# Kernel tuning notes

Hardware: AMD Instinct MI355X
Metric: run time of the kernel (lower is better)

Reference implementation:

```python
import jax, jax.numpy as jnp
import numpy as np

NUM_NODES = 2048
NUM_UNITS = 64
INPUT_DIM = 2
MAX_K = 2  # max_diffusion_step


def setup_inputs() -> dict:
    key = jax.random.key(0)
    ks = jax.random.split(key, 8)
    B, N, U, D = 32, NUM_NODES, NUM_UNITS, INPUT_DIM
    C = D + U                      # input_size after concat = 66
    M = 2 * MAX_K + 1              # num_matrices = 5
    w_scale = 1.0 / np.sqrt(C * M)
    return {
        "inputs": jax.random.normal(ks[0], (B, N * D), dtype=jnp.float32),
        "hx": jax.random.normal(ks[1], (B, N * U), dtype=jnp.float32),
        # row-stochastic-ish random-walk supports (scaled so K hops stay bounded)
        "support0": jax.random.uniform(ks[2], (N, N), dtype=jnp.float32) / N,
        "support1": jax.random.uniform(ks[3], (N, N), dtype=jnp.float32) / N,
        "W_ru": jax.random.normal(ks[4], (C * M, 2 * U), dtype=jnp.float32) * w_scale,
        "b_ru": jnp.full((2 * U,), 1.0, dtype=jnp.float32),   # bias_start=1.0
        "W_c": jax.random.normal(ks[5], (C * M, U), dtype=jnp.float32) * w_scale,
        "b_c": jnp.zeros((U,), dtype=jnp.float32),            # bias_start=0.0
    }


def _gconv(inputs, state, supports, W, b, output_size):
    # inputs: [B, N*D], state: [B, N*U]
    B = inputs.shape[0]
    N = NUM_NODES
    x0 = jnp.concatenate(
        [inputs.reshape(B, N, -1), state.reshape(B, N, -1)], axis=2
    )  # [B, N, C]
    C = x0.shape[2]
    xs = [x0]
    for S in supports:  # Chebyshev-style diffusion per support
        x1 = jnp.einsum("nm,bmc->bnc", S, x0)
        xs.append(x1)
        xk1, xk2 = x1, x0
        for _ in range(2, MAX_K + 1):
            x2 = 2.0 * jnp.einsum("nm,bmc->bnc", S, xk1) - xk2
            xs.append(x2)
            xk1, xk2 = x2, xk1
    M = len(xs)  # num_matrices
    # stack on new leading axis then permute(1,2,3,0): feature-major, matrix-minor
    x = jnp.stack(xs, axis=0).transpose(1, 2, 3, 0).reshape(B * N, C * M)
    out = x @ W + b  # [B*N, output_size]
    return out.reshape(B, N * output_size)


def reference(inputs, hx, support0, support1, W_ru, b_ru, W_c, b_c):
    B = inputs.shape[0]
    N, U = NUM_NODES, NUM_UNITS
    supports = (support0, support1)
    value = jax.nn.sigmoid(_gconv(inputs, hx, supports, W_ru, b_ru, 2 * U))
    value = value.reshape(B, N, 2 * U)
    r = value[..., :U].reshape(B, N * U)
    u = value[..., U:].reshape(B, N * U)
    c = jnp.tanh(_gconv(inputs, r * hx, supports, W_c, b_c, U))
    new_state = u * hx + (1.0 - u) * c
    return new_state
```

## Files before the change

kernel.cpp:

```cpp
#include <hip/hip_runtime.h>
#include <hip/hip_bf16.h>
#include <cstdint>
#include <cstddef>

typedef unsigned short u16;
typedef unsigned char u8;
using f32x4 = __attribute__((ext_vector_type(4))) float;
using s16x8 = __attribute__((ext_vector_type(8))) short;
using s64x2 = __attribute__((ext_vector_type(2))) long;

#define NN 2048
#define BB 32
#define CC 66
#define JREAL 2112
#define JR 2176
#define KF 352
#define SROWS 65536

__device__ __forceinline__ int kperm(int k6) {
  return 16 * ((k6 >> 3) & 3) + 8 * (k6 >> 5) + (k6 & 7);
}

__device__ __forceinline__ float bf2f(u16 u) {
  union { uint32_t i; float f; } v; v.i = ((uint32_t)u) << 16; return v.f;
}
__device__ __forceinline__ u16 f2bf(float f) {
  union { float f; uint32_t i; } v; v.f = f;
  uint32_t x = v.i;
  x += 0x7fffu + ((x >> 16) & 1u);
  return (u16)(x >> 16);
}
__device__ __forceinline__ u8 f2e4m3(float x) {
  union { float f; uint32_t i; } v; v.f = x;
  uint32_t s = (v.i >> 24) & 0x80u;
  float a = fabsf(x);
  if (a >= 464.0f) return (u8)(s | 0x7Eu);
  if (a < 0.015625f) {
    int q = (int)rintf(a * 512.0f);
    return (u8)(s | (uint32_t)q);
  }
  union { float f; uint32_t i; } u; u.f = a;
  uint32_t lsb = (u.i >> 20) & 1u;
  u.i += 0x0007FFFFu + lsb;
  int e = (int)(u.i >> 23) - 127;
  uint32_t m = (u.i >> 20) & 7u;
  return (u8)(s | ((uint32_t)(e + 7) << 3) | m);
}

__device__ __forceinline__ void async_cp16(const u8* g, u8* l) {
  __builtin_amdgcn_global_load_lds(
      (const __attribute__((address_space(1))) unsigned int*)g,
      (__attribute__((address_space(3))) unsigned int*)l, 16, 0, 0);
}
__device__ __forceinline__ void async_cp16u(const u16* g, u16* l) {
  __builtin_amdgcn_global_load_lds(
      (const __attribute__((address_space(1))) unsigned int*)g,
      (__attribute__((address_space(3))) unsigned int*)l, 16, 0, 0);
}

template <int EPI>
__global__ __launch_bounds__(512, 2) void gemm_f8(
    const u8* __restrict__ A0, const u8* __restrict__ A1,
    const u8* __restrict__ A2, const u8* __restrict__ A3,
    const u8* __restrict__ B0, const u8* __restrict__ B1,
    const u8* __restrict__ B2, const u8* __restrict__ B3,
    void* __restrict__ C0, void* __restrict__ C1,
    void* __restrict__ C2, void* __restrict__ C3,
    int K, int lda, int ldb, int ldout, int mlimit)
{
  __shared__ u8 lds[3 * 24576];

  const int gx = gridDim.x, gy = gridDim.y;
  const int nwg = gx * gy * gridDim.z;
  const int orig = blockIdx.x + gx * (blockIdx.y + gy * blockIdx.z);
  const int cpx = nwg >> 3;
  const int swz = (orig & 7) * cpx + (orig >> 3);
  const int mb = swz % gx;
  const int t1 = swz / gx;
  const int nb = t1 % gy;
  const int zb = t1 / gy;

  const u8* A = (zb == 0) ? A0 : (zb == 1) ? A1 : (zb == 2) ? A2 : A3;
  const u8* B = (zb == 0) ? B0 : (zb == 1) ? B1 : (zb == 2) ? B2 : B3;
  void* Cv    = (zb == 0) ? C0 : (zb == 1) ? C1 : (zb == 2) ? C2 : C3;

  const int tid = threadIdx.x;
  const int wid = tid >> 6;
  const int lane = tid & 63;
  const int m0 = mb * 128;
  const int n0 = nb * 256;
  const int wm = (wid >> 2) * 64;
  const int wn = (wid & 3) * 64;

  const int srow = wid * 16 + (lane >> 2);
  const int sk   = ((lane & 3) ^ ((lane >> 3) & 3)) * 16;
  const u8* gA = A + (size_t)(m0 + srow) * lda + sk;
  const u8* gB = B + (size_t)(n0 + srow) * ldb + sk;
  u8* ldsA  = &lds[wid * 1024];
  u8* ldsB0 = &lds[8192 + wid * 1024];
  u8* ldsB1 = &lds[16384 + wid * 1024];

  const int r16 = lane & 15;
  const int hi = lane >> 4;
  const int rq = (r16 >> 1) & 3;
  const int goff = (hi ^ rq) * 16;
  const int abase = (wm + r16) * 64 + goff;
  const int bbase = 8192 + (wn + r16) * 64 + goff;

  f32x4 acc[4][4] = {};
  const int nt = K >> 6;

#define STAGE(T_, SO_) { const int k0_ = (T_) * 64;                          \
    async_cp16(gA + k0_, ldsA + (SO_));                                      \
    async_cp16(gB + k0_, ldsB0 + (SO_));                                     \
    async_cp16(gB + (size_t)128 * ldb + k0_, ldsB1 + (SO_)); }

  STAGE(0, 0);
  STAGE(1, 24576);
  asm volatile("s_waitcnt vmcnt(3)" ::: "memory");
  __builtin_amdgcn_s_barrier();

  int scur = 0;
  for (int t = 0; t < nt; ++t) {
    const int soff = scur * 24576;
    const bool more = (t + 2) < nt;
    if (more) {
      int sst = scur + 2; if (sst >= 3) sst -= 3;
      STAGE(t + 2, sst * 24576);
    }
    s64x2 af[4], bfr[4];
#pragma unroll
    for (int mi = 0; mi < 4; ++mi)
      af[mi] = *(const s64x2*)&lds[soff + abase + mi * 1024];
#pragma unroll
    for (int ni = 0; ni < 4; ++ni)
      bfr[ni] = *(const s64x2*)&lds[soff + bbase + ni * 1024];
    __builtin_amdgcn_s_setprio(1);
#pragma unroll
    for (int h = 0; h < 2; ++h)
#pragma unroll
      for (int mi = 0; mi < 4; ++mi)
#pragma unroll
        for (int ni = 0; ni < 4; ++ni)
          acc[mi][ni] = __builtin_amdgcn_mfma_f32_16x16x32_fp8_fp8(
              af[mi][h], bfr[ni][h], acc[mi][ni], 0, 0, 0);
    __builtin_amdgcn_s_setprio(0);
    if (more) { asm volatile("s_waitcnt vmcnt(3)" ::: "memory"); }
    else      { asm volatile("s_waitcnt vmcnt(0)" ::: "memory"); }
    __builtin_amdgcn_s_barrier();
    scur = (scur + 1 == 3) ? 0 : scur + 1;
  }
#undef STAGE

  const int lr = (lane >> 4) * 4;
  const int lc = lane & 15;

  if (EPI == 5) {
    u16* tl = (u16*)lds;
    u16* xc = (u16*)Cv;
#pragma unroll
    for (int half = 0; half < 2; ++half) {
      __syncthreads();
      if ((wn >> 7) == half) {
#pragma unroll
        for (int mi = 0; mi < 4; ++mi)
#pragma unroll
          for (int ni = 0; ni < 4; ++ni) {
            const int np = (wn & 127) + ni * 16 + lc;
#pragma unroll
            for (int r = 0; r < 4; ++r) {
              const int j = wm + mi * 16 + lr + r;
              tl[np * 130 + j] = f2bf(acc[mi][ni][r] * 0.00390625f);
            }
          }
      }
      __syncthreads();
      for (int p = 0; p < 32; ++p) {
        const int idx = p * 512 + tid;
        const int jj = idx & 127;
        const int np = idx >> 7;
        const int j = m0 + jj;
        if (j < JREAL) {
          const int b = j / CC;
          const int c = j - b * CC;
          const int ng = n0 + half * 128 + np;
          xc[((size_t)b * NN + ng) * KF + (size_t)(zb + 1) * CC + c] =
              tl[np * 130 + jj];
        }
      }
    }
  } else {
#pragma unroll
    for (int mi = 0; mi < 4; ++mi)
#pragma unroll
      for (int ni = 0; ni < 4; ++ni) {
        const int colg = n0 + wn + ni * 16 + lc;
#pragma unroll
        for (int r = 0; r < 4; ++r) {
          const int rowg = m0 + wm + mi * 16 + lr + r;
          if (rowg < mlimit) {
            if (EPI == 0) {
              ((u16*)Cv)[(size_t)rowg * ldout + colg] =
                  f2bf(acc[mi][ni][r] * 0.00390625f);
            } else {
              float v = acc[mi][ni][r] * 0.0078125f -
                        ((rowg == colg) ? 256.0f : 0.0f);
              const int cpk = (colg & ~63) + kperm(colg & 63);
              ((u8*)Cv)[(size_t)rowg * ldout + cpk] = f2e4m3(v);
            }
          }
        }
      }
  }
}

__global__ __launch_bounds__(512, 2) void gemm_f8T(
    const u8* __restrict__ A0, const u8* __restrict__ A1,
    const u8* __restrict__ B0, const u8* __restrict__ B1,
    u8* __restrict__ C0, u8* __restrict__ C1,
    int K, int lda, int ldb, int ldout)
{
  __shared__ u8 lds[3 * 16384];

  const int gx = gridDim.x, gy = gridDim.y;
  const int nwg = gx * gy * gridDim.z;
  const int orig = blockIdx.x + gx * (blockIdx.y + gy * blockIdx.z);
  const int cpx = nwg >> 3;
  const int swz = (orig & 7) * cpx + (orig >> 3);
  const int mb = swz % gx;
  const int t1 = swz / gx;
  const int nb = t1 % gy;
  const int zb = t1 / gy;

  const u8* A = zb ? A1 : A0;
  const u8* B = zb ? B1 : B0;
  u8* C = zb ? C1 : C0;

  const int tid = threadIdx.x;
  const int wid = tid >> 6;
  const int lane = tid & 63;
  const int m0 = mb * 128;
  const int n0 = nb * 128;
  const int wm = (wid >> 2) * 64;
  const int wn = (wid & 3) * 32;

  const int srow = wid * 16 + (lane >> 2);
  const int sk   = ((lane & 3) ^ ((lane >> 3) & 3)) * 16;
  const u8* gA = A + (size_t)(m0 + srow) * lda + sk;
  const u8* gB = B + (size_t)(n0 + srow) * ldb + sk;
  u8* ldsA = &lds[wid * 1024];
  u8* ldsB = &lds[8192 + wid * 1024];

  const int r16 = lane & 15;
  const int hi = lane >> 4;
  const int rq = (r16 >> 1) & 3;
  const int goff = (hi ^ rq) * 16;
  const int abase = (wm + r16) * 64 + goff;
  const int bbase = 8192 + (wn + r16) * 64 + goff;

  f32x4 acc[4][2] = {};
  const int nt = K >> 6;

#define STAGE(T_, SO_) { const int k0_ = (T_) * 64;                          \
    async_cp16(gA + k0_, ldsA + (SO_));                                      \
    async_cp16(gB + k0_, ldsB + (SO_)); }

  STAGE(0, 0);
  STAGE(1, 16384);
  asm volatile("s_waitcnt vmcnt(2)" ::: "memory");
  __builtin_amdgcn_s_barrier();

  int scur = 0;
  for (int t = 0; t < nt; ++t) {
    const int soff = scur * 16384;
    const bool more = (t + 2) < nt;
    if (more) {
      int sst = scur + 2; if (sst >= 3) sst -= 3;
      STAGE(t + 2, sst * 16384);
    }
    s64x2 af[4], bfr[2];
#pragma unroll
    for (int mi = 0; mi < 4; ++mi)
      af[mi] = *(const s64x2*)&lds[soff + abase + mi * 1024];
#pragma unroll
    for (int ni = 0; ni < 2; ++ni)
      bfr[ni] = *(const s64x2*)&lds[soff + bbase + ni * 1024];
    __builtin_amdgcn_s_setprio(1);
#pragma unroll
    for (int h = 0; h < 2; ++h)
#pragma unroll
      for (int mi = 0; mi < 4; ++mi)
#pragma unroll
        for (int ni = 0; ni < 2; ++ni)
          acc[mi][ni] = __builtin_amdgcn_mfma_f32_16x16x32_fp8_fp8(
              af[mi][h], bfr[ni][h], acc[mi][ni], 0, 0, 0);
    __builtin_amdgcn_s_setprio(0);
    if (more) { asm volatile("s_waitcnt vmcnt(2)" ::: "memory"); }
    else      { asm volatile("s_waitcnt vmcnt(0)" ::: "memory"); }
    __builtin_amdgcn_s_barrier();
    scur = (scur + 1 == 3) ? 0 : scur + 1;
  }
#undef STAGE

  const int lr = (lane >> 4) * 4;
  const int lc = lane & 15;
#pragma unroll
  for (int mi = 0; mi < 4; ++mi)
#pragma unroll
    for (int ni = 0; ni < 2; ++ni) {
      const int colg = n0 + wn + ni * 16 + lc;
      const int cpk = (colg & ~63) + kperm(colg & 63);
#pragma unroll
      for (int r = 0; r < 4; ++r) {
        const int rowg = m0 + wm + mi * 16 + lr + r;
        float v = acc[mi][ni][r] * 0.0078125f -
                  ((rowg == colg) ? 256.0f : 0.0f);
        C[(size_t)rowg * ldout + cpk] = f2e4m3(v);
      }
    }
}

template <int EPI>
__global__ __launch_bounds__(256) void gemm_dense(
    const u16* __restrict__ A, const u16* __restrict__ B, u16* __restrict__ C,
    const float* __restrict__ bias,
    int K, int lda, int ldb, int ldout, int nstore)
{
  __shared__ u16 At[128 * 32];
  __shared__ u16 Bt[128 * 32];
  const int nwg = gridDim.x;
  const int orig = blockIdx.x;
  const int cpx = nwg >> 3;
  const int swz = (orig & 7) * cpx + (orig >> 3);
  const int mb = swz;

  const int tid = threadIdx.x;
  const int wid = tid >> 6;
  const int lane = tid & 63;
  const int m0 = mb * 128;
  const int wm = (wid >> 1) * 64;
  const int wn = (wid & 1) * 64;
  const int rA = lane >> 2;
  const int kA = ((lane & 3) ^ ((lane >> 3) & 3)) * 8;

  f32x4 acc[4][4] = {};

  const int c0 = wid * 2, c1 = wid * 2 + 1;
  const u16* gA0 = A + (size_t)(m0 + c0 * 16 + rA) * lda + kA;
  const u16* gA1 = A + (size_t)(m0 + c1 * 16 + rA) * lda + kA;
  const u16* gB0 = B + (size_t)(c0 * 16 + rA) * ldb + kA;
  const u16* gB1 = B + (size_t)(c1 * 16 + rA) * ldb + kA;

  for (int k0 = 0; k0 < K; k0 += 32) {
    async_cp16u(gA0 + k0, &At[c0 * 512]);
    async_cp16u(gA1 + k0, &At[c1 * 512]);
    async_cp16u(gB0 + k0, &Bt[c0 * 512]);
    async_cp16u(gB1 + k0, &Bt[c1 * 512]);
    __syncthreads();
    s16x8 af[4], bfr[4];
    const int r16 = lane & 15;
    const int cswz = ((lane >> 4) ^ ((r16 >> 1) & 3)) << 3;
#pragma unroll
    for (int mi = 0; mi < 4; ++mi)
      af[mi] = *(const s16x8*)&At[(wm + mi * 16 + r16) * 32 + cswz];
#pragma unroll
    for (int ni = 0; ni < 4; ++ni)
      bfr[ni] = *(const s16x8*)&Bt[(wn + ni * 16 + r16) * 32 + cswz];
#pragma unroll
    for (int mi = 0; mi < 4; ++mi)
#pragma unroll
      for (int ni = 0; ni < 4; ++ni)
        acc[mi][ni] = __builtin_amdgcn_mfma_f32_16x16x32_bf16(af[mi], bfr[ni], acc[mi][ni], 0, 0, 0);
    __syncthreads();
  }

  const int lr = (lane >> 4) * 4;
  const int lc = lane & 15;
#pragma unroll
  for (int mi = 0; mi < 4; ++mi) {
#pragma unroll
    for (int ni = 0; ni < 4; ++ni) {
      const int colg = wn + ni * 16 + lc;
#pragma unroll
      for (int r = 0; r < 4; ++r) {
        const int rowg = m0 + wm + mi * 16 + lr + r;
        float v = acc[mi][ni][r];
        if (EPI == 2) { v += bias[colg]; v = 1.0f / (1.0f + __expf(-v)); }
        if (EPI == 3) { v += bias[colg]; v = tanhf(v); }
        if (colg < nstore)
          C[(size_t)rowg * ldout + colg] = f2bf(v);
      }
    }
  }
}

__global__ __launch_bounds__(256) void cvt_S(const float* __restrict__ Sa,
                                             const float* __restrict__ Sb,
                                             u8* __restrict__ Sha, u8* __restrict__ Shb,
                                             u8* __restrict__ Sta, u8* __restrict__ Stb) {
  __shared__ u8 tile[64 * 68];
  const float* S = blockIdx.z ? Sb : Sa;
  u8* Sh = blockIdx.z ? Shb : Sha;
  u8* St = blockIdx.z ? Stb : Sta;
  const int c0 = blockIdx.x * 64;
  const int r0 = blockIdx.y * 64;
  const int t = threadIdx.x;
#pragma unroll
  for (int p = 0; p < 4; ++p) {
    const int idx = p * 256 + t;
    const int r = idx >> 4;
    const int c4 = (idx & 15) * 4;
    float4 v = *reinterpret_cast<const float4*>(S + (size_t)(r0 + r) * NN + c0 + c4);
    union { u8 b[4]; uint32_t w; } o;
    o.b[0] = f2e4m3(v.x * 256.0f); o.b[1] = f2e4m3(v.y * 256.0f);
    o.b[2] = f2e4m3(v.z * 256.0f); o.b[3] = f2e4m3(v.w * 256.0f);
    *reinterpret_cast<uint32_t*>(Sh + (size_t)(r0 + r) * NN + c0 + kperm(c4)) = o.w;
    *reinterpret_cast<uint32_t*>(&tile[r * 68 + c4]) = o.w;
  }
  __syncthreads();
  const int cc = t >> 2;
#pragma unroll
  for (int half = 0; half < 2; ++half) {
    const int j = (t & 3) * 2 + half;
    union { u8 b[8]; uint64_t w; } buf;
#pragma unroll
    for (int i = 0; i < 8; ++i) buf.b[i] = tile[(j * 8 + i) * 68 + cc];
    const int npos = 16 * (j & 3) + 8 * (j >> 2);
    *reinterpret_cast<uint64_t*>(St + (size_t)(c0 + cc) * NN + r0 + npos) = buf.w;
  }
}

__global__ __launch_bounds__(256) void build_wt(const float* __restrict__ W,
                                                u16* __restrict__ Wt, int ocols) {
  int t = blockIdx.x * 256 + threadIdx.x;
  if (t >= 128 * KF) return;
  int o = t / KF, kf = t - o * KF;
  float v = 0.0f;
  if (kf < 330 && o < ocols) {
    int m = kf / CC, c = kf - m * CC;
    v = W[(size_t)(c * 5 + m) * ocols + o];
  }
  Wt[t] = f2bf(v);
}

__global__ __launch_bounds__(256) void pack_x0(const float* __restrict__ inputs,
                                               const float* __restrict__ hx,
                                               const u16* __restrict__ ru,
                                               u8* __restrict__ X0t,
                                               u16* __restrict__ xcat, int useR) {
  __shared__ u16 tile[128 * 76];
  const int n0 = blockIdx.x * 128;
  const int b = blockIdx.y;
  const int t = threadIdx.x;
#pragma unroll
  for (int p = 0; p < 8; ++p) {
    const int idx = p * 256 + t;
    const int n = idx >> 4;
    const int u4 = (idx & 15) * 4;
    float4 v = *reinterpret_cast<const float4*>(
        hx + (size_t)b * (NN * 64) + (size_t)(n0 + n) * 64 + u4);
    if (useR) {
      ushort4 rv = *reinterpret_cast<const ushort4*>(
          ru + ((size_t)b * NN + n0 + n) * 128 + u4);
      v.x *= bf2f(rv.x); v.y *= bf2f(rv.y); v.z *= bf2f(rv.z); v.w *= bf2f(rv.w);
    }
    ushort4 o;
    o.x = f2bf(v.x); o.y = f2bf(v.y); o.z = f2bf(v.z); o.w = f2bf(v.w);
    *reinterpret_cast<ushort4*>(&tile[n * 76 + u4]) = o;
  }
  __syncthreads();
#pragma unroll
  for (int p = 0; p < 33; ++p) {
    const int idx = p * 256 + t;
    const int c = idx >> 7;
    const int n = idx & 127;
    float val;
    if (c < 2) val = inputs[(size_t)b * (NN * 2) + (size_t)(n0 + n) * 2 + c];
    else       val = bf2f(tile[n * 76 + (c - 2)]);
    const int np = (n & ~63) + kperm(n & 63);
    X0t[(size_t)(b * CC + c) * NN + n0 + np] = f2e4m3(val);
  }
#pragma unroll
  for (int p = 0; p < 17; ++p) {
    const int idx = p * 256 + t;
    if (idx < 128 * 33) {
      const int n = idx / 33;
      const int pr = idx - n * 33;
      const int col = pr * 2;
      u16 v0, v1;
      if (col == 0) {
        v0 = f2bf(inputs[(size_t)b * (NN * 2) + (size_t)(n0 + n) * 2 + 0]);
        v1 = f2bf(inputs[(size_t)b * (NN * 2) + (size_t)(n0 + n) * 2 + 1]);
      } else {
        v0 = tile[n * 76 + (col - 2)];
        v1 = tile[n * 76 + (col - 1)];
      }
      ushort2 o2; o2.x = v0; o2.y = v1;
      *reinterpret_cast<ushort2*>(
          xcat + ((size_t)b * NN + n0 + n) * KF + col) = o2;
    }
  }
}

__global__ __launch_bounds__(256) void final_k(const float* __restrict__ hx,
                                               const u16* __restrict__ ru,
                                               const u16* __restrict__ cd,
                                               float* __restrict__ out) {
  size_t t = (size_t)blockIdx.x * 256 + threadIdx.x;
  int u = (int)(t & 63);
  size_t s = t >> 6;
  float ug = bf2f(ru[s * 128 + 64 + u]);
  float cv = bf2f(cd[s * 64 + u]);
  float h = hx[t];
  out[t] = ug * h + (1.0f - ug) * cv;
}

extern "C" void kernel_launch(void* const* d_in, const int* in_sizes, int n_in,
                              void* d_out, int out_size, void* d_ws, size_t ws_size,
                              hipStream_t stream) {
  const float* inputs = (const float*)d_in[0];
  const float* hx     = (const float*)d_in[1];
  const float* S0     = (const float*)d_in[2];
  const float* S1     = (const float*)d_in[3];
  const float* Wru    = (const float*)d_in[4];
  const float* bru    = (const float*)d_in[5];
  const float* Wc     = (const float*)d_in[6];
  const float* bc     = (const float*)d_in[7];
  float* out = (float*)d_out;

  u8* ws8 = (u8*)d_ws;
  u8* S0h = ws8;
  u8* S1h = S0h + (size_t)NN * NN;
  u8* X0t = S1h + (size_t)NN * NN;
  u16* xcat = (u16*)(X0t + (size_t)JR * NN);
  u16* Wtru = xcat + (size_t)SROWS * KF;
  u16* Wtc  = Wtru + (size_t)128 * KF;
  u16* ru   = Wtc + (size_t)128 * KF;
  u16* cd   = ru + (size_t)SROWS * 128;
  u8* S0t = (u8*)xcat;
  u8* S1t = S0t + (size_t)NN * NN;
  u8* T0 = (u8*)d_out;
  u8* T1 = T0 + (size_t)NN * NN;

  dim3 b256(256);
  dim3 b512(512);
  cvt_S<<<dim3(NN / 64, NN / 64, 2), b256, 0, stream>>>(S0, S1, S0h, S1h, S0t, S1t);
  build_wt<<<dim3((128 * KF + 255) / 256), b256, 0, stream>>>(Wru, Wtru, 128);
  build_wt<<<dim3((128 * KF + 255) / 256), b256, 0, stream>>>(Wc, Wtc, 64);

  gemm_f8T<<<dim3(NN / 128, NN / 128, 2), b512, 0, stream>>>(
      S0h, S1h, S0t, S1t, T0, T1, NN, NN, NN, NN);

  const dim3 gdiff(JR / 128, NN / 256, 4);
  const dim3 gdense(SROWS / 128);
  const dim3 gpx0(NN / 128, BB);

  pack_x0<<<gpx0, b256, 0, stream>>>(inputs, hx, (const u16*)nullptr, X0t, xcat, 0);
  gemm_f8<5><<<gdiff, b512, 0, stream>>>(
      X0t, X0t, X0t, X0t,  S0h, T0, S1h, T1,
      (void*)xcat, (void*)xcat, (void*)xcat, (void*)xcat,
      NN, NN, NN, KF, JREAL);
  gemm_dense<2><<<gdense, b256, 0, stream>>>(xcat, Wtru, ru, bru, KF, KF, KF, 128, 128);

  pack_x0<<<gpx0, b256, 0, stream>>>(inputs, hx, ru, X0t, xcat, 1);
  gemm_f8<5><<<gdiff, b512, 0, stream>>>(
      X0t, X0t, X0t, X0t,  S0h, T0, S1h, T1,
      (void*)xcat, (void*)xcat, (void*)xcat, (void*)xcat,
      NN, NN, NN, KF, JREAL);
  gemm_dense<3><<<gdense, b256, 0, stream>>>(xcat, Wtc, cd, bc, KF, KF, KF, 64, 64);

  final_k<<<dim3(SROWS * 64 / 256), b256, 0, stream>>>(hx, ru, cd, out);
}
```

Before: 256.6 us.

## Fold leftover diffusion rows into existing M-tiles instead of an extra tile column

Result: no change. 252.4 us (-1.6%).

```diff
diff --git a/kernel.cpp b/kernel.cpp
--- a/kernel.cpp
+++ b/kernel.cpp
@@ -68,7 +68,7 @@
     void* __restrict__ C2, void* __restrict__ C3,
     int K, int lda, int ldb, int ldout, int mlimit)
 {
-  __shared__ u8 lds[3 * 24576];
+  __shared__ u8 lds[3 * 25600];
 
   const int gx = gridDim.x, gy = gridDim.y;
   const int nwg = gx * gy * gridDim.z;
@@ -92,13 +92,20 @@
   const int wm = (wid >> 2) * 64;
   const int wn = (wid & 3) * 64;
 
+  const bool xtra = (EPI == 5) && (mb < 4);
+  const int xrow0 = 2048 + mb * 16;
+  const bool xw = xtra && (wid == 0);
+  const bool xm = xtra && (wid < 4);
+
   const int srow = wid * 16 + (lane >> 2);
   const int sk   = ((lane & 3) ^ ((lane >> 3) & 3)) * 16;
   const u8* gA = A + (size_t)(m0 + srow) * lda + sk;
   const u8* gB = B + (size_t)(n0 + srow) * ldb + sk;
+  const u8* gAx = A + (size_t)(xrow0 + (lane >> 2)) * lda + sk;
   u8* ldsA  = &lds[wid * 1024];
   u8* ldsB0 = &lds[8192 + wid * 1024];
   u8* ldsB1 = &lds[16384 + wid * 1024];
+  u8* ldsAx = &lds[24576];
 
   const int r16 = lane & 15;
   const int hi = lane >> 4;
@@ -106,35 +113,40 @@
   const int goff = (hi ^ rq) * 16;
   const int abase = (wm + r16) * 64 + goff;
   const int bbase = 8192 + (wn + r16) * 64 + goff;
+  const int xbase = 24576 + r16 * 64 + goff;
 
   f32x4 acc[4][4] = {};
+  f32x4 accx[4] = {};
   const int nt = K >> 6;
 
 #define STAGE(T_, SO_) { const int k0_ = (T_) * 64;                          \
     async_cp16(gA + k0_, ldsA + (SO_));                                      \
     async_cp16(gB + k0_, ldsB0 + (SO_));                                     \
-    async_cp16(gB + (size_t)128 * ldb + k0_, ldsB1 + (SO_)); }
+    async_cp16(gB + (size_t)128 * ldb + k0_, ldsB1 + (SO_));                 \
+    if (xw) async_cp16(gAx + k0_, ldsAx + (SO_)); }
 
   STAGE(0, 0);
-  STAGE(1, 24576);
-  asm volatile("s_waitcnt vmcnt(3)" ::: "memory");
+  STAGE(1, 25600);
+  if (xw) { asm volatile("s_waitcnt vmcnt(4)" ::: "memory"); }
+  else    { asm volatile("s_waitcnt vmcnt(3)" ::: "memory"); }
   __builtin_amdgcn_s_barrier();
 
   int scur = 0;
   for (int t = 0; t < nt; ++t) {
-    const int soff = scur * 24576;
+    const int soff = scur * 25600;
     const bool more = (t + 2) < nt;
     if (more) {
       int sst = scur + 2; if (sst >= 3) sst -= 3;
-      STAGE(t + 2, sst * 24576);
-    }
-    s64x2 af[4], bfr[4];
+      STAGE(t + 2, sst * 25600);
+    }
+    s64x2 af[4], bfr[4], axf;
 #pragma unroll
     for (int mi = 0; mi < 4; ++mi)
       af[mi] = *(const s64x2*)&lds[soff + abase + mi * 1024];
 #pragma unroll
     for (int ni = 0; ni < 4; ++ni)
       bfr[ni] = *(const s64x2*)&lds[soff + bbase + ni * 1024];
+    if (xm) axf = *(const s64x2*)&lds[soff + xbase];
     __builtin_amdgcn_s_setprio(1);
 #pragma unroll
     for (int h = 0; h < 2; ++h)
@@ -144,9 +156,21 @@
         for (int ni = 0; ni < 4; ++ni)
           acc[mi][ni] = __builtin_amdgcn_mfma_f32_16x16x32_fp8_fp8(
               af[mi][h], bfr[ni][h], acc[mi][ni], 0, 0, 0);
+    if (xm) {
+#pragma unroll
+      for (int h = 0; h < 2; ++h)
+#pragma unroll
+        for (int ni = 0; ni < 4; ++ni)
+          accx[ni] = __builtin_amdgcn_mfma_f32_16x16x32_fp8_fp8(
+              axf[h], bfr[ni][h], accx[ni], 0, 0, 0);
+    }
     __builtin_amdgcn_s_setprio(0);
-    if (more) { asm volatile("s_waitcnt vmcnt(3)" ::: "memory"); }
-    else      { asm volatile("s_waitcnt vmcnt(0)" ::: "memory"); }
+    if (more) {
+      if (xw) { asm volatile("s_waitcnt vmcnt(4)" ::: "memory"); }
+      else    { asm volatile("s_waitcnt vmcnt(3)" ::: "memory"); }
+    } else {
+      asm volatile("s_waitcnt vmcnt(0)" ::: "memory");
+    }
     __builtin_amdgcn_s_barrier();
     scur = (scur + 1 == 3) ? 0 : scur + 1;
   }
@@ -158,6 +182,18 @@
   if (EPI == 5) {
     u16* tl = (u16*)lds;
     u16* xc = (u16*)Cv;
+    if (xm) {
+#pragma unroll
+      for (int ni = 0; ni < 4; ++ni) {
+        const int ng = n0 + wn + ni * 16 + lc;
+#pragma unroll
+        for (int r = 0; r < 4; ++r) {
+          const int c = xrow0 + lr + r - 2046;
+          xc[((size_t)31 * NN + ng) * KF + (size_t)(zb + 1) * CC + c] =
+              f2bf(accx[ni][r] * 0.00390625f);
+        }
+      }
+    }
 #pragma unroll
     for (int half = 0; half < 2; ++half) {
       __syncthreads();
@@ -551,7 +587,7 @@
   gemm_f8T<<<dim3(NN / 128, NN / 128, 2), b512, 0, stream>>>(
       S0h, S1h, S0t, S1t, T0, T1, NN, NN, NN, NN);
 
-  const dim3 gdiff(JR / 128, NN / 256, 4);
+  const dim3 gdiff(16, NN / 256, 4);
   const dim3 gdense(SROWS / 128);
   const dim3 gpx0(NN / 128, BB);
 
```
